# Performance work log

Measured on AMD Instinct MI355X. Metric: run time of the kernel, lower is better.

Reference implementation:

```python
import jax, jax.numpy as jnp
import numpy as np

V = 32000   # vocab
E = 512     # hidden_size (d_model)
NH = 8      # num_heads
DH = E // NH
NL = 2      # num_layers
FF = 2048   # TransformerDecoderLayer default dim_feedforward
MAXLEN = 24 # cfg.max_length -> gen_len (no target given)
S, B = 48, 8
TRANS = 14
INIT = TRANS - 2            # tgt = transform[1:-1]
LF = INIT + MAXLEN - 1      # final tgt length after the loop
EPS = 1e-5
NEG = -1e9


def pos_encoding(length, d):
    pos = np.arange(length, dtype=np.float32)[:, None]
    div = np.exp(-np.log(10000.0) * np.arange(0, d, 2, dtype=np.float32) / d)
    pe = np.zeros((length, d), dtype=np.float32)
    pe[:, 0::2] = np.sin(pos * div)
    pe[:, 1::2] = np.cos(pos * div)
    return jnp.asarray(pe)


def setup_inputs() -> dict:
    key = jax.random.key(0)
    ks = jax.random.split(key, 12)
    s = 0.02
    return {
        "enc_outputs": jax.random.normal(ks[0], (S, B, E), jnp.float32),
        "transform": jax.random.randint(ks[1], (TRANS, B), 0, V),
        "tf_ratio": 0,
        "emb_table": jax.random.normal(ks[2], (V, E), jnp.float32) * s,
        "sa_w": jax.random.normal(ks[3], (NL, 3 * E, E), jnp.float32) * s,
        "sa_b": jnp.zeros((NL, 3 * E), jnp.float32),
        "sa_ow": jax.random.normal(ks[4], (NL, E, E), jnp.float32) * s,
        "sa_ob": jnp.zeros((NL, E), jnp.float32),
        "ca_w": jax.random.normal(ks[5], (NL, 3 * E, E), jnp.float32) * s,
        "ca_b": jnp.zeros((NL, 3 * E), jnp.float32),
        "ca_ow": jax.random.normal(ks[6], (NL, E, E), jnp.float32) * s,
        "ca_ob": jnp.zeros((NL, E), jnp.float32),
        "ff1_w": jax.random.normal(ks[7], (NL, FF, E), jnp.float32) * s,
        "ff1_b": jnp.zeros((NL, FF), jnp.float32),
        "ff2_w": jax.random.normal(ks[8], (NL, E, FF), jnp.float32) * s,
        "ff2_b": jnp.zeros((NL, E), jnp.float32),
        "ln_g": jnp.ones((NL, 3, E), jnp.float32),
        "ln_b": jnp.zeros((NL, 3, E), jnp.float32),
        "out_w": jax.random.normal(ks[9], (V, E), jnp.float32) * s,
        "out_b": jnp.zeros((V,), jnp.float32),
    }


def _ln(x, g, b):
    m = jnp.mean(x, -1, keepdims=True)
    v = jnp.mean((x - m) ** 2, -1, keepdims=True)
    return (x - m) * jax.lax.rsqrt(v + EPS) * g + b


def _mha(q_in, kv_in, w, b, ow, ob, mask):
    # q_in [Lq,B,E], kv_in [Lk,B,E]; PyTorch packed in_proj [3E,E]
    wq, wk, wv = jnp.split(w, 3, 0)
    bq, bk, bv = jnp.split(b, 3, 0)
    proj = lambda x, wm, bm: (x @ wm.T + bm).reshape(x.shape[0], x.shape[1], NH, DH)
    q, k, v = proj(q_in, wq, bq), proj(kv_in, wk, bk), proj(kv_in, wv, bv)
    sc = jnp.einsum('qbhd,kbhd->bhqk', q, k) / np.sqrt(DH).astype(np.float32)
    if mask is not None:
        sc = sc + mask
    a = jax.nn.softmax(sc, -1)
    o = jnp.einsum('bhqk,kbhd->qbhd', a, v).reshape(q_in.shape[0], q_in.shape[1], E)
    return o @ ow.T + ob


def _decoder(x, mem, mask, p):
    # post-norm TransformerDecoderLayer: self-attn -> cross-attn -> relu FFN
    for l in range(NL):
        x = _ln(x + _mha(x, x, p['sa_w'][l], p['sa_b'][l], p['sa_ow'][l], p['sa_ob'][l], mask),
                p['ln_g'][l, 0], p['ln_b'][l, 0])
        x = _ln(x + _mha(x, mem, p['ca_w'][l], p['ca_b'][l], p['ca_ow'][l], p['ca_ob'][l], None),
                p['ln_g'][l, 1], p['ln_b'][l, 1])
        h = jax.nn.relu(x @ p['ff1_w'][l].T + p['ff1_b'][l]) @ p['ff2_w'][l].T + p['ff2_b'][l]
        x = _ln(x + h, p['ln_g'][l, 2], p['ln_b'][l, 2])
    return x


def reference(enc_outputs, transform, tf_ratio, emb_table, sa_w, sa_b, sa_ow, sa_ob,
              ca_w, ca_b, ca_ow, ca_ob, ff1_w, ff1_b, ff2_w, ff2_b, ln_g, ln_b,
              out_w, out_b):
    # tf_ratio == 0 -> no teacher forcing; gen_len = max_length (no target attr)
    p = dict(sa_w=sa_w, sa_b=sa_b, sa_ow=sa_ow, sa_ob=sa_ob, ca_w=ca_w, ca_b=ca_b,
             ca_ow=ca_ow, ca_ob=ca_ob, ff1_w=ff1_w, ff1_b=ff1_b, ff2_w=ff2_w,
             ff2_b=ff2_b, ln_g=ln_g, ln_b=ln_b)
    pe = pos_encoding(MAXLEN, E)
    # causal mask over the fixed-size buffer; padded (future) slots cannot
    # influence valid positions, so full-buffer passes == torch prefix passes.
    mask = jnp.where(jnp.tril(jnp.ones((LF, LF), bool)), 0.0, NEG)
    tgt0 = emb_table[transform[1:-1]] + pe[:INIT][:, None, :]   # [INIT,B,E]
    buf = jnp.zeros((LF, B, E), jnp.float32).at[:INIT].set(tgt0)

    def step(buf, i):
        h = _decoder(buf, enc_outputs, mask, p)
        pos = INIT - 1 + i                        # last valid position
        pred = jnp.argmax(h[pos] @ out_w.T + out_b, axis=-1)   # [B]
        # torch re-embeds the single predicted token -> PE position 0
        emb = emb_table[pred] + pe[0]
        return buf.at[pos + 1].set(emb), None

    buf, _ = jax.lax.scan(step, buf, jnp.arange(MAXLEN - 1))
    h = _decoder(buf, enc_outputs, mask, p)       # final loop iteration's pass
    return h @ out_w.T + out_b                    # dec_outputs [LF,B,V]
```

## Files before the change

kernel.cpp:

```cpp
#include <hip/hip_runtime.h>
#include <hip/hip_bf16.h>
#include <math.h>

#define V    32000
#define E    512
#define NH   8
#define DH   64
#define NL   2
#define FF   2048
#define MAXLEN 24
#define S    48
#define B    8
#define TRANS 14
#define INIT 12
#define LF   35

#define NB   256
#define NT   1024

typedef float f4 __attribute__((ext_vector_type(4)));

__device__ inline float wsum(float v) {
#pragma unroll
  for (int off = 32; off; off >>= 1) v += __shfl_xor(v, off);
  return v;
}
__device__ inline float wmax(float v) {
#pragma unroll
  for (int off = 32; off; off >>= 1) v = fmaxf(v, __shfl_xor(v, off));
  return v;
}

__device__ inline void stc(float* p, float v) {
  __hip_atomic_store(p, v, __ATOMIC_RELAXED, __HIP_MEMORY_SCOPE_AGENT);
}
__device__ inline void stc8(float* p, float x, float y) {
  union { unsigned long long u; float f[2]; } c; c.f[0] = x; c.f[1] = y;
  __hip_atomic_store((unsigned long long*)p, c.u, __ATOMIC_RELAXED, __HIP_MEMORY_SCOPE_AGENT);
}
__device__ inline int ldci(const int* p) {
  return __hip_atomic_load(p, __ATOMIC_RELAXED, __HIP_MEMORY_SCOPE_AGENT);
}
__device__ inline void stci(int* p, int v) {
  __hip_atomic_store(p, v, __ATOMIC_RELAXED, __HIP_MEMORY_SCOPE_AGENT);
}

#define CMB(v, idx, ov, oi) do { if ((ov) > (v) || ((ov) == (v) && (oi) < (idx))) { (v) = (ov); (idx) = (oi); } } while (0)


__global__ void embed_init_k(const int* __restrict__ transform, const float* __restrict__ emb,
                             float* __restrict__ xbuf) {
  int t = blockIdx.x;
  int pos = t >> 3, b = t & 7;
  int tok = transform[(1 + pos) * B + b];
  for (int d = threadIdx.x; d < E; d += blockDim.x) {
    double div = exp(-log(10000.0) * (double)(d & ~1) / (double)E);
    double ang = (double)pos * div;
    float pe = (d & 1) ? (float)cos(ang) : (float)sin(ang);
    xbuf[(size_t)t * E + d] = emb[(size_t)tok * E + d] + pe;
  }
}

template <int K>
__global__ __launch_bounds__(256) void gemm_k(
    const float* __restrict__ x, const float* __restrict__ W, const float* __restrict__ bias,
    int ntok, int nout, int route, int relu,
    float* __restrict__ out0, float* __restrict__ out1, float* __restrict__ out2) {
  constexpr int K4 = K / 4;
  constexpr int J  = K / 256;
  __shared__ float4 xt[8][K4];
  const int tid = threadIdx.x;
  const int lane = tid & 63;
  const int o = blockIdx.x * 4 + (tid >> 6);

  float4 wr[J];
  if (o < nout) {
    const float4* Wr = (const float4*)(W + (size_t)o * K);
#pragma unroll
    for (int j = 0; j < J; ++j) wr[j] = Wr[lane + 64 * j];
  }

  const int ng = ntok >> 3;
  for (int g = 0; g < ng; ++g) {
    if (g) __syncthreads();
    const float4* xg = (const float4*)(x + (size_t)g * 8 * K);
    float4* xf = &xt[0][0];
    for (int i = tid; i < 8 * K4; i += 256) xf[i] = xg[i];
    __syncthreads();
    if (o < nout) {
      float acc[8] = {0, 0, 0, 0, 0, 0, 0, 0};
#pragma unroll
      for (int j = 0; j < J; ++j) {
        float4 w = wr[j];
#pragma unroll
        for (int tt = 0; tt < 8; ++tt) {
          float4 xv = xt[tt][lane + 64 * j];
          acc[tt] += w.x * xv.x + w.y * xv.y + w.z * xv.z + w.w * xv.w;
        }
      }
#pragma unroll
      for (int tt = 0; tt < 8; ++tt) acc[tt] = wsum(acc[tt]);
      if (lane == 0) {
        float bo = bias[o];
#pragma unroll
        for (int tt = 0; tt < 8; ++tt) {
          float v = acc[tt] + bo;
          if (relu) v = fmaxf(v, 0.f);
          int t = g * 8 + tt;
          if (route == 0) {
            out0[(size_t)t * nout + o] = v;
          } else if (route == 1) {
            if (o < E) out0[(size_t)t * E + o] = v;
            else if (o < 2 * E) out1[(size_t)t * E + (o - E)] = v;
            else out2[(size_t)t * E + (o - 2 * E)] = v;
          } else {
            if (o < E) out0[(size_t)t * E + o] = v;
            else out1[(size_t)t * E + (o - E)] = v;
          }
        }
      }
    }
  }
}

__global__ __launch_bounds__(256) void attn_k(
    const float* __restrict__ q, const float* __restrict__ Kc, const float* __restrict__ Vc,
    float* __restrict__ outp, int p0, int nq, int nk_fixed, int causal) {
  const int tid = threadIdx.x;
  const int lane = tid & 63;
  const int u = blockIdx.x * 4 + (tid >> 6);
  if (u >= nq * 64) return;
  const int qi = u >> 6;
  const int r = u & 63;
  const int b = r >> 3, h = r & 7;
  const int nk = causal ? (p0 + qi + 1) : nk_fixed;

  const size_t qoff = (size_t)(qi * B + b) * E + h * DH + lane;
  const float qv = q[qoff];

  float myscore = -INFINITY;
  for (int k = 0; k < nk; ++k) {
    float prod = qv * Kc[(size_t)(k * B + b) * E + h * DH + lane];
    prod = wsum(prod);
    if (lane == k) myscore = prod * 0.125f;
  }
  float m = wmax(myscore);
  float p = (lane < nk) ? expf(myscore - m) : 0.f;
  float denom = wsum(p);
  float a = p / denom;

  float oacc = 0.f;
  for (int k = 0; k < nk; ++k) {
    float ak = __shfl(a, k);
    oacc = fmaf(ak, Vc[(size_t)(k * B + b) * E + h * DH + lane], oacc);
  }
  outp[qoff] = oacc;
}

__global__ __launch_bounds__(256) void add_ln_k(
    const float* __restrict__ xa, const float* __restrict__ xb,
    const float* __restrict__ g, const float* __restrict__ beta,
    float* __restrict__ outp, int ntok) {
  const int tid = threadIdx.x, lane = tid & 63;
  const int t = blockIdx.x * 4 + (tid >> 6);
  if (t >= ntok) return;
  float v[8];
  float s = 0.f;
#pragma unroll
  for (int j = 0; j < 8; ++j) {
    int d = lane + 64 * j;
    v[j] = xa[(size_t)t * E + d] + xb[(size_t)t * E + d];
    s += v[j];
  }
  s = wsum(s);
  float mean = s * (1.f / 512.f);
  float d2 = 0.f;
#pragma unroll
  for (int j = 0; j < 8; ++j) { float dd = v[j] - mean; d2 += dd * dd; }
  d2 = wsum(d2);
  float inv = 1.f / sqrtf(d2 * (1.f / 512.f) + 1e-5f);
#pragma unroll
  for (int j = 0; j < 8; ++j) {
    int d = lane + 64 * j;
    outp[(size_t)t * E + d] = (v[j] - mean) * inv * g[d] + beta[d];
  }
}

#define B_QKV 0
#define B_OW  6144
#define B_CQ  8192
#define B_COW 10240
#define B_FF1 12288
#define B_FF2 20480
#define SW_TOT 28672
#define SLOTS_PER_STEP 23
#define NSTAGE 17

__global__ __launch_bounds__(NT, 1) void decode_persist_k(
    const float* __restrict__ emb,
    const float* __restrict__ sa_w, const float* __restrict__ sa_b,
    const float* __restrict__ sa_ow, const float* __restrict__ sa_ob,
    const float* __restrict__ ca_w, const float* __restrict__ ca_b,
    const float* __restrict__ ca_ow, const float* __restrict__ ca_ob,
    const float* __restrict__ ff1_w, const float* __restrict__ ff1_b,
    const float* __restrict__ ff2_w, const float* __restrict__ ff2_b,
    const float* __restrict__ ln_g, const float* __restrict__ ln_b,
    const float* __restrict__ out_w, const float* __restrict__ out_b,
    float* __restrict__ kself, float* __restrict__ vself,
    const float* __restrict__ kcross, const float* __restrict__ vcross,
    float* __restrict__ arena, float* __restrict__ outp, int* __restrict__ bar) {
  __shared__ __align__(16) float s_w[SW_TOT];
  __shared__ __align__(16) float s_x[8 * E];
  __shared__ __align__(16) float s_raw[8 * E];
  __shared__ __align__(16) float s_q2[64];
  __shared__ __align__(16) float s_attw[64];
  __shared__ __align__(16) float s_part[4][64];
  __shared__ int   s_tok[8];
  __shared__ float s_pv[16][8];
  __shared__ int   s_pi[16][8];

  const int tid  = threadIdx.x;
  const int lane = tid & 63;
  const int wv   = tid >> 6;
  const int bid  = blockIdx.x;

  auto slot = [&](int st, int s) -> float* {
    return arena + ((size_t)st * SLOTS_PER_STEP + s) * 4096;
  };

  auto flg = [&](int s, int j) -> int* { return &bar[(s * 256 + j) * 16]; };

  auto set_flag = [&](int s, int tgt, bool producer) {
    __syncthreads();
    if (producer && tid == 0) stci(flg(s, bid), tgt);
  };
  auto wait_flags = [&](int s, int base, int count, int tgt) {
    if (wv == 0) {
      const int m = count - 1;
      for (;;) {
        bool ok = true;
        for (int f = lane; f < count; f += 64)
          ok &= (ldci(flg(s, base + ((f + bid) & m))) >= tgt);
        if (__all(ok)) break;
        __builtin_amdgcn_s_sleep(12);
      }
    }
    __syncthreads();
  };

  auto stage_raw = [&](const float* src) {
    const float4* s4 = (const float4*)src;
    float4* d4 = (float4*)s_raw;
    for (int k = tid; k < 1024; k += NT) d4[k] = s4[k];
    __syncthreads();
  };
  auto lnstage = [&](int lnidx) {
    if (wv < 8) {
      const float* gg = ln_g + (size_t)lnidx * E;
      const float* be = ln_b + (size_t)lnidx * E;
      float v[8]; float sum = 0.f;
#pragma unroll
      for (int j = 0; j < 8; ++j) {
        int d = lane + 64 * j;
        v[j] = s_x[wv * E + d] + s_raw[wv * E + d];
        sum += v[j];
      }
      sum = wsum(sum);
      float mean = sum * (1.f / 512.f);
      float d2 = 0.f;
#pragma unroll
      for (int j = 0; j < 8; ++j) { float dd = v[j] - mean; d2 += dd * dd; }
      d2 = wsum(d2);
      float inv = 1.f / sqrtf(d2 * (1.f / 512.f) + 1e-5f);
#pragma unroll
      for (int j = 0; j < 8; ++j) {
        int d = lane + 64 * j;
        s_x[wv * E + d] = (v[j] - mean) * inv * gg[d] + be[d];
      }
    }
    __syncthreads();
  };
  auto proj16 = [&](int wbase, const float* srcLDS, const float* biasp, float* dst) {
    int j = wv & 1, b = wv >> 1;
    int r = bid * 2 + j;
    const f4* wp = (const f4*)&s_w[wbase + j * 512];
    f4 w0 = wp[lane], w1 = wp[lane + 64];
    const f4* x4 = (const f4*)(srcLDS + b * E);
    f4 a = w0 * x4[lane] + w1 * x4[lane + 64];
    float acc = a.x + a.y + a.z + a.w;
    acc = wsum(acc);
    if (lane == 0) stc(&dst[b * E + r], acc + biasp[r]);
  };
  auto attn_stage = [&](const float* qsrc, const float* Kbase, const float* Vbase,
                        int nk, float* attdst) {
    const int b = bid >> 3, h = bid & 7;
    if (wv == 0) {
      s_q2[lane] = qsrc[b * E + h * DH + lane];
      float sc = -INFINITY;
      if (lane < nk) {
        const f4* Kr = (const f4*)(Kbase + ((size_t)lane * B + b) * E + h * DH);
        const f4* Qp = (const f4*)s_q2;
        float a0 = 0.f;
#pragma unroll
        for (int u = 0; u < 16; ++u) {
          f4 kv = Kr[u], qq = Qp[u];
          a0 += kv.x * qq.x + kv.y * qq.y + kv.z * qq.z + kv.w * qq.w;
        }
        sc = a0 * 0.125f;
      }
      float m = wmax(sc);
      float e = (lane < nk) ? expf(sc - m) : 0.f;
      float den = wsum(e);
      s_attw[lane] = e / den;
    }
    __syncthreads();
    if (wv < 4) {
      float o = 0.f;
      for (int k = wv; k < nk; k += 4)
        o = fmaf(s_attw[k], Vbase[((size_t)k * B + b) * E + h * DH + lane], o);
      s_part[wv][lane] = o;
    }
    __syncthreads();
    if (wv == 0)
      stc(&attdst[b * E + h * DH + lane],
          s_part[0][lane] + s_part[1][lane] + s_part[2][lane] + s_part[3][lane]);
  };

  {
    auto cprow = [&](const float* src, int dstf) {
      f4* d = (f4*)&s_w[dstf]; const f4* s = (const f4*)src;
      for (int k = tid; k < 128; k += NT) d[k] = s[k];
    };
    for (int l = 0; l < NL; ++l) {
      for (int j = 0; j < 6; ++j)
        cprow(sa_w + ((size_t)l * 1536 + bid * 6 + j) * E, B_QKV + (l * 6 + j) * 512);
      for (int j = 0; j < 2; ++j) {
        cprow(sa_ow + ((size_t)l * 512 + bid * 2 + j) * E, B_OW + (l * 2 + j) * 512);
        cprow(ca_w + ((size_t)l * 1536 + bid * 2 + j) * E, B_CQ + (l * 2 + j) * 512);
        cprow(ca_ow + ((size_t)l * 512 + bid * 2 + j) * E, B_COW + (l * 2 + j) * 512);
      }
      for (int j = 0; j < 8; ++j)
        cprow(ff1_w + ((size_t)l * FF + bid * 8 + j) * E, B_FF1 + (l * 8 + j) * 512);
    }
    const int lf2 = bid >> 7;
    for (int j = 0; j < 4; ++j) {
      f4* d = (f4*)&s_w[B_FF2 + j * 2048];
      const f4* s = (const f4*)(ff2_w + ((size_t)lf2 * 512 + (bid & 127) * 4 + j) * FF);
      for (int k = tid; k < 512; k += NT) d[k] = s[k];
    }
    __syncthreads();
  }

  for (int i = 0; i < MAXLEN - 1; ++i) {
    const int p = INIT + i;
    const int tgt = i + 1;
    float* amax_o = slot(i, 0);

    if (i > 0) wait_flags(16, 0, 256, i);
    {
      int bw = wv & 7;
      float v = -INFINITY; int ix = 0x7fffffff;
      if (i == 0) {
        const float2* row = (const float2*)(outp + ((size_t)(INIT - 1) * B + bw) * V);
        for (int jj = lane; jj < V / 2; jj += 64) {
          float2 t = row[jj];
          CMB(v, ix, t.x, 2 * jj);
          CMB(v, ix, t.y, 2 * jj + 1);
        }
      } else {
        const float2* ap = (const float2*)slot(i - 1, 0);
#pragma unroll
        for (int t = 0; t < 4; ++t) {
          int e = lane * 4 + t;
          float2 pr = ap[e * 8 + bw];
          CMB(v, ix, pr.x, (int)pr.y);
        }
      }
#pragma unroll
      for (int off = 1; off < 64; off <<= 1) {
        float ov = __shfl_xor(v, off); int oi = __shfl_xor(ix, off);
        CMB(v, ix, ov, oi);
      }
      if (lane == 0 && wv < 8) s_tok[bw] = ix;
      __syncthreads();
      int b = tid >> 7, d0 = (tid & 127) * 4;
      int tok = s_tok[b];
      float4 ev = *(const float4*)(emb + (size_t)tok * E + d0);
      s_x[b * E + d0]     = ev.x;
      s_x[b * E + d0 + 1] = ev.y + 1.0f;
      s_x[b * E + d0 + 2] = ev.z;
      s_x[b * E + d0 + 3] = ev.w + 1.0f;
      __syncthreads();
    }

    for (int l = 0; l < NL; ++l) {
      const int sb = l * 8;
      float* Lb    = slot(i, 1 + l * 11);
      float* q_s   = Lb;
      float* att_s = Lb + 4096;
      float* raw_s = Lb + 8192;
      float* q_c   = Lb + 12288;
      float* att_c = Lb + 16384;
      float* raw_c = Lb + 20480;
      float* hb    = Lb + 24576;
      float* yb    = Lb + 40960;

      if (wv < 12) {
        int j = wv >> 1, bg = (wv & 1) * 4;
        int r = bid * 6 + j, sec = r >> 9, off = r & 511;
        const f4* wp = (const f4*)&s_w[B_QKV + (l * 6 + j) * 512];
        f4 w0 = wp[lane], w1 = wp[lane + 64];
        float bias = sa_b[(size_t)l * 1536 + r];
        for (int b = bg; b < bg + 4; ++b) {
          const f4* x4 = (const f4*)&s_x[b * E];
          f4 a = w0 * x4[lane] + w1 * x4[lane + 64];
          float acc = a.x + a.y + a.z + a.w;
          acc = wsum(acc);
          if (lane == 0) {
            acc += bias;
            if (sec == 0) stc(&q_s[b * E + off], acc);
            else if (sec == 1) stc(&kself[((size_t)(l * LF + p) * B + b) * E + off], acc);
            else stc(&vself[((size_t)(l * LF + p) * B + b) * E + off], acc);
          }
        }
      }
      set_flag(sb + 0, tgt, true);
      wait_flags(sb + 0, 0, 256, tgt);
      if (bid < 64)
        attn_stage(q_s, kself + (size_t)l * LF * B * E, vself + (size_t)l * LF * B * E,
                   p + 1, att_s);
      set_flag(sb + 1, tgt, bid < 64);
      wait_flags(sb + 1, 0, 64, tgt);
      stage_raw(att_s);
      proj16(B_OW + l * 1024, s_raw, sa_ob + (size_t)l * E, raw_s);
      set_flag(sb + 2, tgt, true);
      wait_flags(sb + 2, 0, 256, tgt);
      stage_raw(raw_s);
      lnstage(l * 3 + 0);
      proj16(B_CQ + l * 1024, s_x, ca_b + (size_t)l * 3 * E, q_c);
      set_flag(sb + 3, tgt, true);
      wait_flags(sb + 3, 0, 256, tgt);
      if (bid < 64)
        attn_stage(q_c, kcross + (size_t)l * S * B * E, vcross + (size_t)l * S * B * E,
                   S, att_c);
      set_flag(sb + 4, tgt, bid < 64);
      wait_flags(sb + 4, 0, 64, tgt);
      stage_raw(att_c);
      proj16(B_COW + l * 1024, s_raw, ca_ob + (size_t)l * E, raw_c);
      set_flag(sb + 5, tgt, true);
      wait_flags(sb + 5, 0, 256, tgt);
      stage_raw(raw_c);
      lnstage(l * 3 + 1);
      {
        int j = wv >> 1, bg = (wv & 1) * 4;
        int r = bid * 8 + j;
        const f4* wp = (const f4*)&s_w[B_FF1 + (l * 8 + j) * 512];
        f4 w0 = wp[lane], w1 = wp[lane + 64];
        float bias = ff1_b[(size_t)l * FF + r];
        for (int b = bg; b < bg + 4; ++b) {
          const f4* x4 = (const f4*)&s_x[b * E];
          f4 a = w0 * x4[lane] + w1 * x4[lane + 64];
          float acc = a.x + a.y + a.z + a.w;
          acc = wsum(acc);
          if (lane == 0) stc(&hb[b * FF + r], fmaxf(acc + bias, 0.f));
        }
      }
      set_flag(sb + 6, tgt, true);
      wait_flags(sb + 6, 0, 256, tgt);
      if ((bid >> 7) == l) {
        int b = wv >> 1, j0 = (wv & 1) * 2;
        int r0 = (bid & 127) * 4;
        const f4* h4 = (const f4*)(hb + b * FF);
        f4 hv[8];
#pragma unroll
        for (int j = 0; j < 8; ++j) hv[j] = h4[j * 64 + lane];
#pragma unroll
        for (int jr = 0; jr < 2; ++jr) {
          int rl = j0 + jr;
          const f4* wp = (const f4*)&s_w[B_FF2 + rl * 2048];
          float acc = 0.f;
#pragma unroll
          for (int j = 0; j < 8; ++j) {
            f4 w = wp[j * 64 + lane];
            acc += w.x * hv[j].x + w.y * hv[j].y + w.z * hv[j].z + w.w * hv[j].w;
          }
          acc = wsum(acc);
          if (lane == 0)
            stc(&yb[b * E + r0 + rl], acc + ff2_b[(size_t)l * 512 + r0 + rl]);
        }
      }
      set_flag(sb + 7, tgt, (bid >> 7) == l);
      wait_flags(sb + 7, l * 128, 128, tgt);
      stage_raw(yb);
      lnstage(l * 3 + 2);
    }

    {
      const int grp = lane >> 3, sub = lane & 7;
      const int idx = wv * 8 + grp;
      const bool valid = idx < 125;
      const int r = bid * 125 + idx;
      float acc[8] = {0, 0, 0, 0, 0, 0, 0, 0};
      if (valid) {
        const f4* wrow = (const f4*)(out_w + (size_t)r * E);
#pragma unroll
        for (int half = 0; half < 2; ++half) {
          f4 w8[8];
#pragma unroll
          for (int j = 0; j < 8; ++j) w8[j] = wrow[(half * 8 + j) * 8 + sub];
#pragma unroll
          for (int b = 0; b < 8; ++b) {
            const f4* x4 = (const f4*)&s_x[b * E];
            float a = 0.f;
#pragma unroll
            for (int j = 0; j < 8; ++j) {
              f4 xx = x4[(half * 8 + j) * 8 + sub];
              a += w8[j].x * xx.x + w8[j].y * xx.y + w8[j].z * xx.z + w8[j].w * xx.w;
            }
            acc[b] += a;
          }
        }
#pragma unroll
        for (int b = 0; b < 8; ++b) {
          acc[b] += __shfl_xor(acc[b], 1);
          acc[b] += __shfl_xor(acc[b], 2);
          acc[b] += __shfl_xor(acc[b], 4);
        }
        if (sub == 0) {
          float bo = out_b[r];
#pragma unroll
          for (int b = 0; b < 8; ++b) {
            acc[b] += bo;
            outp[((size_t)p * B + b) * V + r] = acc[b];
          }
        }
      }
#pragma unroll
      for (int b = 0; b < 8; ++b) {
        float v = (valid && sub == 0) ? acc[b] : -INFINITY;
        int ix = (valid && sub == 0) ? r : 0x7fffffff;
#pragma unroll
        for (int off = 1; off < 64; off <<= 1) {
          float ov = __shfl_xor(v, off); int oi = __shfl_xor(ix, off);
          CMB(v, ix, ov, oi);
        }
        if (lane == 0) { s_pv[wv][b] = v; s_pi[wv][b] = ix; }
      }
      __syncthreads();
      if (wv == 0) {
        int b = lane & 7, w2 = lane >> 3;
        float v = s_pv[w2][b]; int ix = s_pi[w2][b];
        float v2 = s_pv[w2 + 8][b]; int ix2 = s_pi[w2 + 8][b];
        CMB(v, ix, v2, ix2);
#pragma unroll
        for (int off = 8; off < 64; off <<= 1) {
          float ov = __shfl_xor(v, off); int oi = __shfl_xor(ix, off);
          CMB(v, ix, ov, oi);
        }
        if (lane < 8) stc8(&amax_o[(size_t)(bid * 8 + lane) * 2], v, (float)ix);
      }
    }
    set_flag(16, tgt, true);
  }
}

extern "C" void kernel_launch(void* const* d_in, const int* in_sizes, int n_in,
                              void* d_out, int out_size, void* d_ws, size_t ws_size,
                              hipStream_t stream) {
  const float* enc       = (const float*)d_in[0];
  const int*   transform = (const int*)d_in[1];
  const float* emb       = (const float*)d_in[3];
  const float* sa_w  = (const float*)d_in[4];
  const float* sa_b  = (const float*)d_in[5];
  const float* sa_ow = (const float*)d_in[6];
  const float* sa_ob = (const float*)d_in[7];
  const float* ca_w  = (const float*)d_in[8];
  const float* ca_b  = (const float*)d_in[9];
  const float* ca_ow = (const float*)d_in[10];
  const float* ca_ob = (const float*)d_in[11];
  const float* ff1_w = (const float*)d_in[12];
  const float* ff1_b = (const float*)d_in[13];
  const float* ff2_w = (const float*)d_in[14];
  const float* ff2_b = (const float*)d_in[15];
  const float* ln_g  = (const float*)d_in[16];
  const float* ln_b  = (const float*)d_in[17];
  const float* out_w = (const float*)d_in[18];
  const float* out_b = (const float*)d_in[19];
  float* out = (float*)d_out;

  const size_t SELF_SZ  = (size_t)LF * B * E;
  const size_t CROSS_SZ = (size_t)S * B * E;
  const size_t ARENA_SZ = (size_t)(MAXLEN - 1) * SLOTS_PER_STEP * 4096;
  const size_t FLAG_SZ  = (size_t)NSTAGE * 256 * 16;
  float* ws     = (float*)d_ws;
  float* xbuf   = ws;
  float* kself  = xbuf + (size_t)INIT * B * E;
  float* vself  = kself + NL * SELF_SZ;
  float* kcross = vself + NL * SELF_SZ;
  float* vcross = kcross + NL * CROSS_SZ;
  float* arena  = vcross + NL * CROSS_SZ;
  int*   bar    = (int*)(arena + ARENA_SZ);
  float* act1   = (float*)(bar + FLAG_SZ);
  float* act2   = act1 + 96 * E;
  float* act3   = act2 + 96 * E;
  float* ffb    = act3 + 96 * E;

  hipMemsetAsync(bar, 0, FLAG_SZ * 4, stream);

  embed_init_k<<<INIT * B, 128, 0, stream>>>(transform, emb, xbuf);

  for (int l = 0; l < NL; ++l) {
    gemm_k<E><<<(2 * E) / 4, 256, 0, stream>>>(
        enc, ca_w + ((size_t)l * 3 * E + E) * E, ca_b + (size_t)l * 3 * E + E,
        S * B, 2 * E, 2, 0, kcross + l * CROSS_SZ, vcross + l * CROSS_SZ, nullptr);
  }

  {
    const int p0 = 0, nq = INIT, ntok = nq * B;
    const float* xin = xbuf;
    for (int l = 0; l < NL; ++l) {
      const float* x = (l == 0) ? xin : act1;
      gemm_k<E><<<(3 * E) / 4, 256, 0, stream>>>(
          x, sa_w + (size_t)l * 3 * E * E, sa_b + (size_t)l * 3 * E, ntok, 3 * E, 1, 0,
          act2, kself + l * SELF_SZ, vself + l * SELF_SZ);
      attn_k<<<nq * 16, 256, 0, stream>>>(act2, kself + l * SELF_SZ, vself + l * SELF_SZ,
                                          act3, p0, nq, 0, 1);
      gemm_k<E><<<E / 4, 256, 0, stream>>>(
          act3, sa_ow + (size_t)l * E * E, sa_ob + (size_t)l * E, ntok, E, 0, 0, act2, nullptr, nullptr);
      add_ln_k<<<(ntok + 3) / 4, 256, 0, stream>>>(
          x, act2, ln_g + (size_t)l * 3 * E, ln_b + (size_t)l * 3 * E, act1, ntok);
      gemm_k<E><<<E / 4, 256, 0, stream>>>(
          act1, ca_w + (size_t)l * 3 * E * E, ca_b + (size_t)l * 3 * E, ntok, E, 0, 0, act2, nullptr, nullptr);
      attn_k<<<nq * 16, 256, 0, stream>>>(act2, kcross + l * CROSS_SZ, vcross + l * CROSS_SZ,
                                          act3, p0, nq, S, 0);
      gemm_k<E><<<E / 4, 256, 0, stream>>>(
          act3, ca_ow + (size_t)l * E * E, ca_ob + (size_t)l * E, ntok, E, 0, 0, act2, nullptr, nullptr);
      add_ln_k<<<(ntok + 3) / 4, 256, 0, stream>>>(
          act1, act2, ln_g + (size_t)l * 3 * E + E, ln_b + (size_t)l * 3 * E + E, act1, ntok);
      gemm_k<E><<<FF / 4, 256, 0, stream>>>(
          act1, ff1_w + (size_t)l * FF * E, ff1_b + (size_t)l * FF, ntok, FF, 0, 1, ffb, nullptr, nullptr);
      gemm_k<FF><<<E / 4, 256, 0, stream>>>(
          ffb, ff2_w + (size_t)l * E * FF, ff2_b + (size_t)l * E, ntok, E, 0, 0, act2, nullptr, nullptr);
      add_ln_k<<<(ntok + 3) / 4, 256, 0, stream>>>(
          act1, act2, ln_g + (size_t)l * 3 * E + 2 * E, ln_b + (size_t)l * 3 * E + 2 * E, act1, ntok);
    }
    gemm_k<E><<<V / 4, 256, 0, stream>>>(
        act1, out_w, out_b, ntok, V, 0, 0, out, nullptr, nullptr);
  }

  decode_persist_k<<<NB, NT, 0, stream>>>(
      emb, sa_w, sa_b, sa_ow, sa_ob, ca_w, ca_b, ca_ow, ca_ob,
      ff1_w, ff1_b, ff2_w, ff2_b, ln_g, ln_b, out_w, out_b,
      kself, vself, kcross, vcross, arena, out, bar);
}
```

Before: 5.071 ms.

## Fuse QKV and cross-Q projections into attention blocks, removing grid barriers

The 64 attention blocks now compute their own head's Q/K/V (and the cross-attention Q) directly from global weights, then run attention locally using the fresh K/V from LDS. This removes two grid-wide flag barriers per layer, so 13 stages replace 17 per step, and drops the per-block QKV and cross-Q weight copies from LDS. Outputs are also gathered in LDS and written as paired 8-byte stores instead of scattered scalar stores, and the spin sleep is shortened. The cost is that 64 blocks now stream 1536+512 weight rows each from global memory every step instead of using weights spread across 256 blocks' LDS, which puts more serial work on fewer CUs.

```diff
diff --git a/kernel.cpp b/kernel.cpp
--- a/kernel.cpp
+++ b/kernel.cpp
@@ -186,15 +186,13 @@
   }
 }
 
-#define B_QKV 0
-#define B_OW  6144
-#define B_CQ  8192
-#define B_COW 10240
-#define B_FF1 12288
-#define B_FF2 20480
-#define SW_TOT 28672
-#define SLOTS_PER_STEP 23
-#define NSTAGE 17
+#define B_OW  0
+#define B_COW 2048
+#define B_FF1 4096
+#define B_FF2 12288
+#define SW_TOT 20480
+#define SLOTS_PER_STEP 19
+#define NSTAGE 13
 
 __global__ __launch_bounds__(NT, 1) void decode_persist_k(
     const float* __restrict__ emb,
@@ -212,12 +210,19 @@
   __shared__ __align__(16) float s_w[SW_TOT];
   __shared__ __align__(16) float s_x[8 * E];
   __shared__ __align__(16) float s_raw[8 * E];
-  __shared__ __align__(16) float s_q2[64];
+  __shared__ __align__(16) float s_qh[64];
+  __shared__ __align__(16) float s_kh[64];
+  __shared__ __align__(16) float s_vh[64];
   __shared__ __align__(16) float s_attw[64];
   __shared__ __align__(16) float s_part[4][64];
+  __shared__ float s_col[16];
+  __shared__ float s_f1[8][8];
+  __shared__ float s_c2[8][4];
   __shared__ int   s_tok[8];
   __shared__ float s_pv[16][8];
   __shared__ int   s_pi[16][8];
+  __shared__ float s_rv[NT];
+  __shared__ int   s_ri[NT];
 
   const int tid  = threadIdx.x;
   const int lane = tid & 63;
@@ -227,7 +232,6 @@
   auto slot = [&](int st, int s) -> float* {
     return arena + ((size_t)st * SLOTS_PER_STEP + s) * 4096;
   };
-
   auto flg = [&](int s, int j) -> int* { return &bar[(s * 256 + j) * 16]; };
 
   auto set_flag = [&](int s, int tgt, bool producer) {
@@ -242,7 +246,7 @@
         for (int f = lane; f < count; f += 64)
           ok &= (ldci(flg(s, base + ((f + bid) & m))) >= tgt);
         if (__all(ok)) break;
-        __builtin_amdgcn_s_sleep(12);
+        __builtin_amdgcn_s_sleep(8);
       }
     }
     __syncthreads();
@@ -280,26 +284,27 @@
     }
     __syncthreads();
   };
-  auto proj16 = [&](int wbase, const float* srcLDS, const float* biasp, float* dst) {
+  auto proj16v = [&](int wbase, const float* biasp, float* dst) {
     int j = wv & 1, b = wv >> 1;
     int r = bid * 2 + j;
     const f4* wp = (const f4*)&s_w[wbase + j * 512];
     f4 w0 = wp[lane], w1 = wp[lane + 64];
-    const f4* x4 = (const f4*)(srcLDS + b * E);
+    const f4* x4 = (const f4*)(s_raw + b * E);
     f4 a = w0 * x4[lane] + w1 * x4[lane + 64];
     float acc = a.x + a.y + a.z + a.w;
     acc = wsum(acc);
-    if (lane == 0) stc(&dst[b * E + r], acc + biasp[r]);
+    if (lane == 0) s_col[b * 2 + j] = acc + biasp[r];
+    __syncthreads();
+    if (tid < 8) stc8(&dst[tid * E + bid * 2], s_col[tid * 2], s_col[tid * 2 + 1]);
   };
-  auto attn_stage = [&](const float* qsrc, const float* Kbase, const float* Vbase,
-                        int nk, float* attdst) {
-    const int b = bid >> 3, h = bid & 7;
+  auto attn_core = [&](int b, int h, const float* Kbase, const float* Vbase,
+                       int nk, int self, float* attdst) {
     if (wv == 0) {
-      s_q2[lane] = qsrc[b * E + h * DH + lane];
       float sc = -INFINITY;
       if (lane < nk) {
-        const f4* Kr = (const f4*)(Kbase + ((size_t)lane * B + b) * E + h * DH);
-        const f4* Qp = (const f4*)s_q2;
+        const f4* Kr = (self && lane == nk - 1) ? (const f4*)s_kh
+                       : (const f4*)(Kbase + ((size_t)lane * B + b) * E + h * DH);
+        const f4* Qp = (const f4*)s_qh;
         float a0 = 0.f;
 #pragma unroll
         for (int u = 0; u < 16; ++u) {
@@ -316,14 +321,20 @@
     __syncthreads();
     if (wv < 4) {
       float o = 0.f;
-      for (int k = wv; k < nk; k += 4)
-        o = fmaf(s_attw[k], Vbase[((size_t)k * B + b) * E + h * DH + lane], o);
+      for (int k = wv; k < nk; k += 4) {
+        const float* vp = (self && k == nk - 1) ? s_vh
+                          : &Vbase[((size_t)k * B + b) * E + h * DH];
+        o = fmaf(s_attw[k], vp[lane], o);
+      }
       s_part[wv][lane] = o;
     }
     __syncthreads();
-    if (wv == 0)
-      stc(&attdst[b * E + h * DH + lane],
-          s_part[0][lane] + s_part[1][lane] + s_part[2][lane] + s_part[3][lane]);
+    if (wv == 0) {
+      float tot = s_part[0][lane] + s_part[1][lane] + s_part[2][lane] + s_part[3][lane];
+      float lo = __shfl(tot, 2 * (lane & 31));
+      float hi = __shfl(tot, 2 * (lane & 31) + 1);
+      if (lane < 32) stc8(&attdst[b * E + h * DH + 2 * lane], lo, hi);
+    }
   };
 
   {
@@ -332,11 +343,8 @@
       for (int k = tid; k < 128; k += NT) d[k] = s[k];
     };
     for (int l = 0; l < NL; ++l) {
-      for (int j = 0; j < 6; ++j)
-        cprow(sa_w + ((size_t)l * 1536 + bid * 6 + j) * E, B_QKV + (l * 6 + j) * 512);
       for (int j = 0; j < 2; ++j) {
         cprow(sa_ow + ((size_t)l * 512 + bid * 2 + j) * E, B_OW + (l * 2 + j) * 512);
-        cprow(ca_w + ((size_t)l * 1536 + bid * 2 + j) * E, B_CQ + (l * 2 + j) * 512);
         cprow(ca_ow + ((size_t)l * 512 + bid * 2 + j) * E, B_COW + (l * 2 + j) * 512);
       }
       for (int j = 0; j < 8; ++j)
@@ -356,7 +364,7 @@
     const int tgt = i + 1;
     float* amax_o = slot(i, 0);
 
-    if (i > 0) wait_flags(16, 0, 256, i);
+    if (i > 0) wait_flags(12, 0, 256, i);
     {
       int bw = wv & 7;
       float v = -INFINITY; int ix = 0x7fffffff;
@@ -394,61 +402,73 @@
     }
 
     for (int l = 0; l < NL; ++l) {
-      const int sb = l * 8;
-      float* Lb    = slot(i, 1 + l * 11);
-      float* q_s   = Lb;
-      float* att_s = Lb + 4096;
-      float* raw_s = Lb + 8192;
-      float* q_c   = Lb + 12288;
-      float* att_c = Lb + 16384;
-      float* raw_c = Lb + 20480;
-      float* hb    = Lb + 24576;
-      float* yb    = Lb + 40960;
-
-      if (wv < 12) {
-        int j = wv >> 1, bg = (wv & 1) * 4;
-        int r = bid * 6 + j, sec = r >> 9, off = r & 511;
-        const f4* wp = (const f4*)&s_w[B_QKV + (l * 6 + j) * 512];
-        f4 w0 = wp[lane], w1 = wp[lane + 64];
-        float bias = sa_b[(size_t)l * 1536 + r];
-        for (int b = bg; b < bg + 4; ++b) {
+      const int sb = l * 6;
+      float* Lb    = slot(i, 1 + l * 9);
+      float* att_s = Lb;
+      float* raw_s = Lb + 4096;
+      float* att_c = Lb + 8192;
+      float* raw_c = Lb + 12288;
+      float* hb    = Lb + 16384;
+      float* yb    = Lb + 32768;
+
+      if (bid < 64) {
+        const int b = bid >> 3, h = bid & 7;
+#pragma unroll
+        for (int t = 0; t < 12; ++t) {
+          int idx = wv * 12 + t;
+          int sec = idx >> 6, o = idx & 63;
+          const f4* wp = (const f4*)(sa_w + ((size_t)l * 1536 + sec * 512 + h * 64 + o) * E);
           const f4* x4 = (const f4*)&s_x[b * E];
-          f4 a = w0 * x4[lane] + w1 * x4[lane + 64];
+          f4 a = wp[lane] * x4[lane] + wp[lane + 64] * x4[lane + 64];
           float acc = a.x + a.y + a.z + a.w;
           acc = wsum(acc);
           if (lane == 0) {
-            acc += bias;
-            if (sec == 0) stc(&q_s[b * E + off], acc);
-            else if (sec == 1) stc(&kself[((size_t)(l * LF + p) * B + b) * E + off], acc);
-            else stc(&vself[((size_t)(l * LF + p) * B + b) * E + off], acc);
+            acc += sa_b[(size_t)l * 1536 + sec * 512 + h * 64 + o];
+            if (sec == 0) s_qh[o] = acc;
+            else if (sec == 1) s_kh[o] = acc;
+            else s_vh[o] = acc;
           }
         }
-      }
-      set_flag(sb + 0, tgt, true);
-      wait_flags(sb + 0, 0, 256, tgt);
-      if (bid < 64)
-        attn_stage(q_s, kself + (size_t)l * LF * B * E, vself + (size_t)l * LF * B * E,
-                   p + 1, att_s);
-      set_flag(sb + 1, tgt, bid < 64);
-      wait_flags(sb + 1, 0, 64, tgt);
+        __syncthreads();
+        if (tid < 16)
+          ((float4*)(kself + ((size_t)(l * LF + p) * B + b) * E + h * DH))[tid] =
+              ((float4*)s_kh)[tid];
+        else if (tid < 32)
+          ((float4*)(vself + ((size_t)(l * LF + p) * B + b) * E + h * DH))[tid - 16] =
+              ((float4*)s_vh)[tid - 16];
+        attn_core(b, h, kself + (size_t)l * LF * B * E, vself + (size_t)l * LF * B * E,
+                  p + 1, 1, att_s);
+      }
+      set_flag(sb + 0, tgt, bid < 64);
+      wait_flags(sb + 0, 0, 64, tgt);
       stage_raw(att_s);
-      proj16(B_OW + l * 1024, s_raw, sa_ob + (size_t)l * E, raw_s);
-      set_flag(sb + 2, tgt, true);
-      wait_flags(sb + 2, 0, 256, tgt);
+      proj16v(B_OW + l * 1024, sa_ob + (size_t)l * E, raw_s);
+      set_flag(sb + 1, tgt, true);
+      wait_flags(sb + 1, 0, 256, tgt);
       stage_raw(raw_s);
       lnstage(l * 3 + 0);
-      proj16(B_CQ + l * 1024, s_x, ca_b + (size_t)l * 3 * E, q_c);
+      if (bid < 64) {
+        const int b = bid >> 3, h = bid & 7;
+#pragma unroll
+        for (int t = 0; t < 4; ++t) {
+          int o = wv * 4 + t;
+          const f4* wp = (const f4*)(ca_w + ((size_t)l * 1536 + h * 64 + o) * E);
+          const f4* x4 = (const f4*)&s_x[b * E];
+          f4 a = wp[lane] * x4[lane] + wp[lane + 64] * x4[lane + 64];
+          float acc = a.x + a.y + a.z + a.w;
+          acc = wsum(acc);
+          if (lane == 0) s_qh[o] = acc + ca_b[(size_t)l * 1536 + h * 64 + o];
+        }
+        __syncthreads();
+        attn_core(b, h, kcross + (size_t)l * S * B * E, vcross + (size_t)l * S * B * E,
+                  S, 0, att_c);
+      }
+      set_flag(sb + 2, tgt, bid < 64);
+      wait_flags(sb + 2, 0, 64, tgt);
+      stage_raw(att_c);
+      proj16v(B_COW + l * 1024, ca_ob + (size_t)l * E, raw_c);
       set_flag(sb + 3, tgt, true);
       wait_flags(sb + 3, 0, 256, tgt);
-      if (bid < 64)
-        attn_stage(q_c, kcross + (size_t)l * S * B * E, vcross + (size_t)l * S * B * E,
-                   S, att_c);
-      set_flag(sb + 4, tgt, bid < 64);
-      wait_flags(sb + 4, 0, 64, tgt);
-      stage_raw(att_c);
-      proj16(B_COW + l * 1024, s_raw, ca_ob + (size_t)l * E, raw_c);
-      set_flag(sb + 5, tgt, true);
-      wait_flags(sb + 5, 0, 256, tgt);
       stage_raw(raw_c);
       lnstage(l * 3 + 1);
       {
@@ -462,11 +482,16 @@
           f4 a = w0 * x4[lane] + w1 * x4[lane + 64];
           float acc = a.x + a.y + a.z + a.w;
           acc = wsum(acc);
-          if (lane == 0) stc(&hb[b * FF + r], fmaxf(acc + bias, 0.f));
-        }
-      }
-      set_flag(sb + 6, tgt, true);
-      wait_flags(sb + 6, 0, 256, tgt);
+          if (lane == 0) s_f1[b][j] = fmaxf(acc + bias, 0.f);
+        }
+      }
+      __syncthreads();
+      if (tid < 32) {
+        int b = tid >> 2, q = tid & 3;
+        stc8(&hb[b * FF + bid * 8 + q * 2], s_f1[b][q * 2], s_f1[b][q * 2 + 1]);
+      }
+      set_flag(sb + 4, tgt, true);
+      wait_flags(sb + 4, 0, 256, tgt);
       if ((bid >> 7) == l) {
         int b = wv >> 1, j0 = (wv & 1) * 2;
         int r0 = (bid & 127) * 4;
@@ -485,12 +510,16 @@
             acc += w.x * hv[j].x + w.y * hv[j].y + w.z * hv[j].z + w.w * hv[j].w;
           }
           acc = wsum(acc);
-          if (lane == 0)
-            stc(&yb[b * E + r0 + rl], acc + ff2_b[(size_t)l * 512 + r0 + rl]);
-        }
-      }
-      set_flag(sb + 7, tgt, (bid >> 7) == l);
-      wait_flags(sb + 7, l * 128, 128, tgt);
+          if (lane == 0) s_c2[b][rl] = acc + ff2_b[(size_t)l * 512 + r0 + rl];
+        }
+        __syncthreads();
+        if (tid < 16) {
+          int b2 = tid >> 1, q = tid & 1;
+          stc8(&yb[b2 * E + r0 + q * 2], s_c2[b2][q * 2], s_c2[b2][q * 2 + 1]);
+        }
+      }
+      set_flag(sb + 5, tgt, (bid >> 7) == l);
+      wait_flags(sb + 5, l * 128, 128, tgt);
       stage_raw(yb);
       lnstage(l * 3 + 2);
     }
@@ -560,7 +589,7 @@
         if (lane < 8) stc8(&amax_o[(size_t)(bid * 8 + lane) * 2], v, (float)ix);
       }
     }
-    set_flag(16, tgt, true);
+    set_flag(12, tgt, true);
   }
 }
 
```

Measured after the change: 5.665 ms. 11.7% more time.
